# Optimization experiments

Hardware: AMD Instinct MI355X
Metric: run time of the kernel (lower is better)

The kernel has to match this reference:

```python
import jax, jax.numpy as jnp
import numpy as np

B, N, C = 2, 2048, 256
H_DIM, W_DIM = 64, 176


def _lin_init(k, fan_in, shape):
    return jax.random.normal(k, shape, dtype=jnp.float32) * (1.0 / np.sqrt(fan_in))


def setup_inputs() -> dict:
    key = jax.random.key(0)
    ks = jax.random.split(key, 12)
    # gaussian_data: (B, N, 14); positions [:3], sigma_x at 5, sigma_y at 6, weight at 12
    z = jax.random.uniform(ks[0], (B, N), minval=1.0, maxval=40.0)
    x = jax.random.uniform(ks[1], (B, N), minval=-0.6, maxval=0.6) * z
    y = jax.random.uniform(ks[2], (B, N), minval=-0.4, maxval=0.4) * z
    g = jax.random.normal(ks[3], (B, N, 14), dtype=jnp.float32)
    g = g.at[..., 0].set(x).at[..., 1].set(y).at[..., 2].set(z)
    g = g.at[..., 5].set(jax.random.uniform(ks[4], (B, N), minval=5.0, maxval=50.0))
    g = g.at[..., 6].set(jax.random.uniform(ks[5], (B, N), minval=5.0, maxval=50.0))
    g = g.at[..., 12].set(jax.random.uniform(ks[6], (B, N), minval=0.5, maxval=1.5))
    # pinhole intrinsic: fx=fy=1000, cx=880, cy=320
    intrinsic = jnp.array([[1000.0, 0.0, 880.0], [0.0, 1000.0, 320.0], [0.0, 0.0, 1.0]], dtype=jnp.float32)
    pk = jax.random.split(ks[7], 5)
    return {
        "gaussian_data": g,
        "intrinsic": intrinsic,
        "enc_w1": _lin_init(pk[0], 14, (14, 64)), "enc_b1": jnp.zeros((64,), jnp.float32),
        "enc_w2": _lin_init(pk[1], 64, (64, 128)), "enc_b2": jnp.zeros((128,), jnp.float32),
        "enc_w3": _lin_init(pk[2], 128, (128, C)), "enc_b3": jnp.zeros((C,), jnp.float32),
        "ft_w1": _lin_init(pk[3], C, (C, C)), "ft_b1": jnp.zeros((C,), jnp.float32),
        "ft_w2": _lin_init(pk[4], C, (C, C)), "ft_b2": jnp.zeros((C,), jnp.float32),
        "H": H_DIM, "W": W_DIM,
    }


def reference(gaussian_data, intrinsic, enc_w1, enc_b1, enc_w2, enc_b2, enc_w3, enc_b3,
              ft_w1, ft_b1, ft_w2, ft_b2, H, W):
    # Encoder MLP (dropout = identity in eval): (B,N,14) -> (B,N,C)
    h = jax.nn.relu(gaussian_data @ enc_w1 + enc_b1)
    h = jax.nn.relu(h @ enc_w2 + enc_b2)
    feats = h @ enc_w3 + enc_b3
    # feature_transform inside GaussianRadarProjection
    feats_t = jax.nn.relu(feats @ ft_w1 + ft_b1) @ ft_w2 + ft_b2  # (B,N,C)

    pos = gaussian_data[..., :3]                      # (B,N,3)
    valid = pos[..., 2] > 0.1                         # (B,N)
    proj = jnp.einsum('ij,bnj->bni', intrinsic, pos)  # (B,N,3)
    pts2d = proj[..., :2] / (proj[..., 2:3] + 1e-6)   # (B,N,2)
    scale_x = W / intrinsic[0, 2] / 2
    scale_y = H / intrinsic[1, 2] / 2
    px = pts2d[..., 0] * scale_x                      # (B,N)
    py = pts2d[..., 1] * scale_y
    inb = (px >= 0) & (px < W) & (py >= 0) & (py < H)
    mask = valid & inb                                # (B,N)

    sx = jnp.maximum(gaussian_data[..., 5] * scale_x, 1.0)  # (B,N)
    sy = jnp.maximum(gaussian_data[..., 6] * scale_y, 1.0)
    w = gaussian_data[..., 12]                               # (B,N)

    xg = jnp.arange(W, dtype=jnp.float32)
    yg = jnp.arange(H, dtype=jnp.float32)
    dx2 = ((xg[None, None, :] - px[..., None]) / sx[..., None]) ** 2  # (B,N,W)
    dy2 = ((yg[None, None, :] - py[..., None]) / sy[..., None]) ** 2  # (B,N,H)
    dist = dy2[..., :, None] + dx2[..., None, :]                      # (B,N,H,W)
    gw = jnp.exp(-0.5 * dist) * w[..., None, None]
    gw = gw * (dist < 9.0).astype(gw.dtype) * mask[..., None, None].astype(gw.dtype)

    density = jnp.sum(gw, axis=1)[:, None]                             # (B,1,H,W)
    feature_map = jnp.einsum('bnc,bnhw->bchw', feats_t, gw)            # (B,C,H,W)
    avg_sigma = (sx + sy) / 2                                          # (B,N)
    uncertainty = jnp.sum(gw * avg_sigma[..., None, None], axis=1)[:, None]

    density = jnp.clip(density, 1e-6)
    return feature_map / density, uncertainty / density, density
```

## Files before the change

### kernel.cpp

```cpp
#include <hip/hip_runtime.h>
#include <cstdint>
#include <cstddef>

#define B_ 2
#define N_ 2048
#define C_ 256
#define H_ 64
#define W_ 176
#define TW 16
#define NTX 11
#define NYB 32
#define NTILES2 (B_*NYB*NTX)
#define NSUB 8
#define SUBCAP 256
#define SA 260
#define FS 40
#define CSTRIDE 16

typedef unsigned short ushort_t;
typedef short bf16x8 __attribute__((ext_vector_type(8)));
typedef float f32x4  __attribute__((ext_vector_type(4)));

__device__ __forceinline__ short f2bf(float f)
{
    unsigned u = __float_as_uint(f);
    return (short)((u + 0x7FFFu + ((u >> 16) & 1u)) >> 16);
}

__global__ __launch_bounds__(256)
void prep_kernel(const float* __restrict__ w3f, const float* __restrict__ fw1f,
                 const float* __restrict__ fw2f,
                 short* __restrict__ wt3, short* __restrict__ wt4,
                 short* __restrict__ wt5, int* __restrict__ counts)
{
    const int gid = blockIdx.x * 256 + threadIdx.x;
    for (int c = gid; c < NTILES2 * NSUB * CSTRIDE; c += 65536) counts[c] = 0;
    for (int e = gid; e < 163840; e += 65536) {
        if (e < 32768) {
            const int k = e >> 8, n = e & 255;
            wt3[n * 128 + k] = f2bf(w3f[e]);
        } else if (e < 98304) {
            const int e2 = e - 32768;
            const int k = e2 >> 8, n = e2 & 255;
            wt4[n * 256 + k] = f2bf(fw1f[e2]);
        } else {
            const int e2 = e - 98304;
            const int k = e2 >> 8, n = e2 & 255;
            wt5[n * 256 + k] = f2bf(fw2f[e2]);
        }
    }
}

template<int K>
__device__ __forceinline__ void mfma_acc(const short* __restrict__ wt,
                                         const float* actIn, f32x4 (&acc)[2],
                                         int wv_, int quad, int ln15)
{
    bf16x8 wreg[K / 16];
#pragma unroll
    for (int ks = 0; ks < K / 32; ++ks) {
        const int kb = ks * 32 + quad * 8;
#pragma unroll
        for (int tt = 0; tt < 2; ++tt) {
            const int n0 = (wv_ * 2 + tt) * 16;
            wreg[ks * 2 + tt] = *(const bf16x8*)&wt[(size_t)(n0 + ln15) * K + kb];
        }
    }
#pragma unroll
    for (int ks = 0; ks < K / 32; ++ks) {
        const int kb = ks * 32 + quad * 8;
        const float4 a0 = *(const float4*)&actIn[ln15 * SA + kb];
        const float4 a1 = *(const float4*)&actIn[ln15 * SA + kb + 4];
        bf16x8 af = { f2bf(a0.x), f2bf(a0.y), f2bf(a0.z), f2bf(a0.w),
                      f2bf(a1.x), f2bf(a1.y), f2bf(a1.z), f2bf(a1.w) };
#pragma unroll
        for (int tt = 0; tt < 2; ++tt)
            acc[tt] = __builtin_amdgcn_mfma_f32_16x16x32_bf16(af, wreg[ks * 2 + tt],
                                                              acc[tt], 0, 0, 0);
    }
}

__global__ __launch_bounds__(512, 4)
void pb_mlp_kernel(const float* __restrict__ g, const float* __restrict__ intr,
                   const float* __restrict__ w1, const float* __restrict__ b1,
                   const float* __restrict__ w2, const float* __restrict__ b2,
                   const short* __restrict__ wt3, const float* __restrict__ b3,
                   const short* __restrict__ wt4, const float* __restrict__ fb1,
                   const short* __restrict__ wt5, const float* __restrict__ fb2,
                   ushort_t* __restrict__ ftb,
                   float* __restrict__ pp, int* __restrict__ counts,
                   ushort_t* __restrict__ lists)
{
    __shared__ __align__(16) float A_[16 * SA];
    __shared__ __align__(16) float Bb[16 * SA];
    const int tid = threadIdx.x;

    if (blockIdx.x < 256) {
        const int row0 = blockIdx.x * 16;
        const int lane = tid & 63;
        const int wv_  = tid >> 6;
        const int quad = lane >> 4;
        const int ln15 = lane & 15;

        if (tid < 224) {
            const int k = tid / 16, m = tid % 16;
            A_[m * SA + k] = g[(size_t)(row0 + m) * 14 + k];
        }
        __syncthreads();

        {
            const int col = tid & 63;
            const int m0  = (tid >> 6) * 2;
            float acc[2];
            const float bv = b1[col];
            acc[0] = bv; acc[1] = bv;
#pragma unroll
            for (int k = 0; k < 14; ++k) {
                const float wv = w1[k * 64 + col];
                acc[0] = fmaf(A_[(m0 + 0) * SA + k], wv, acc[0]);
                acc[1] = fmaf(A_[(m0 + 1) * SA + k], wv, acc[1]);
            }
            Bb[(m0 + 0) * SA + col] = fmaxf(acc[0], 0.f);
            Bb[(m0 + 1) * SA + col] = fmaxf(acc[1], 0.f);
        }
        __syncthreads();

        {
            const int col = tid & 127;
            const int m0  = (tid >> 7) * 4;
            float acc[4];
            const float bv = b2[col];
#pragma unroll
            for (int r = 0; r < 4; ++r) acc[r] = bv;
#pragma unroll 4
            for (int kq = 0; kq < 16; ++kq) {
                float wv[4];
#pragma unroll
                for (int jj = 0; jj < 4; ++jj) wv[jj] = w2[(4 * kq + jj) * 128 + col];
#pragma unroll
                for (int r = 0; r < 4; ++r) {
                    const float4 a4 = *(const float4*)&Bb[(m0 + r) * SA + 4 * kq];
                    acc[r] = fmaf(a4.x, wv[0], acc[r]);
                    acc[r] = fmaf(a4.y, wv[1], acc[r]);
                    acc[r] = fmaf(a4.z, wv[2], acc[r]);
                    acc[r] = fmaf(a4.w, wv[3], acc[r]);
                }
            }
#pragma unroll
            for (int r = 0; r < 4; ++r)
                A_[(m0 + r) * SA + col] = fmaxf(acc[r], 0.f);
        }
        __syncthreads();

        {
            f32x4 acc[2] = {{0,0,0,0},{0,0,0,0}};
            mfma_acc<128>(wt3, A_, acc, wv_, quad, ln15);
            __syncthreads();
#pragma unroll
            for (int tt = 0; tt < 2; ++tt) {
                const int n = (wv_ * 2 + tt) * 16 + ln15;
                const float bv = b3[n];
#pragma unroll
                for (int r = 0; r < 4; ++r)
                    Bb[(quad * 4 + r) * SA + n] = acc[tt][r] + bv;
            }
        }
        __syncthreads();

        {
            f32x4 acc[2] = {{0,0,0,0},{0,0,0,0}};
            mfma_acc<256>(wt4, Bb, acc, wv_, quad, ln15);
            __syncthreads();
#pragma unroll
            for (int tt = 0; tt < 2; ++tt) {
                const int n = (wv_ * 2 + tt) * 16 + ln15;
                const float bv = fb1[n];
#pragma unroll
                for (int r = 0; r < 4; ++r)
                    A_[(quad * 4 + r) * SA + n] = fmaxf(acc[tt][r] + bv, 0.f);
            }
        }
        __syncthreads();

        {
            f32x4 acc[2] = {{0,0,0,0},{0,0,0,0}};
            mfma_acc<256>(wt5, A_, acc, wv_, quad, ln15);
#pragma unroll
            for (int tt = 0; tt < 2; ++tt) {
                const int n = (wv_ * 2 + tt) * 16 + ln15;
                const float bv = fb2[n];
#pragma unroll
                for (int r = 0; r < 4; ++r)
                    ftb[(size_t)(row0 + quad * 4 + r) * 256 + n] =
                        (ushort_t)f2bf(acc[tt][r] + bv);
            }
        }
        return;
    }

    const int sub = (blockIdx.x - 256) & (NSUB - 1);
    const int i = (blockIdx.x - 256) * 16 + (tid >> 5);
    const int j = tid & 31;
    const float* gi = g + (size_t)i * 14;
    const float x = gi[0], y = gi[1], z = gi[2];
    const float s5 = gi[5], s6 = gi[6], wv = gi[12];
    const float k00 = intr[0], k01 = intr[1], k02 = intr[2];
    const float k10 = intr[3], k11 = intr[4], k12 = intr[5];
    const float k20 = intr[6], k21 = intr[7], k22 = intr[8];
    const float projx = k00 * x + k01 * y + k02 * z;
    const float projy = k10 * x + k11 * y + k12 * z;
    const float projz = k20 * x + k21 * y + k22 * z;
    const float inv = 1.f / (projz + 1e-6f);
    const float scale_x = (float)W_ / k02 * 0.5f;
    const float scale_y = (float)H_ / k12 * 0.5f;
    const float px = projx * inv * scale_x;
    const float py = projy * inv * scale_y;
    const bool valid = z > 0.1f;
    const bool inb = (px >= 0.f) && (px < (float)W_) && (py >= 0.f) && (py < (float)H_);
    const bool mask = valid && inb;
    const float sx = fmaxf(s5 * scale_x, 1.f);
    const float sy = fmaxf(s6 * scale_y, 1.f);
    if (j == 0) {
        float4* o = (float4*)(pp + (size_t)i * 8);
        o[0] = make_float4(px, py, 1.f / sx, 1.f / sy);
        o[1] = make_float4(wv, 0.5f * (sx + sy), 0.f, 0.f);
    }
    if (!mask) return;
    const float rx = 3.f * sx, ry = 3.f * sy;
    const int ymin = max(0, (int)floorf(py - ry));
    const int ymax = min(H_ - 1, (int)ceilf(py + ry));
    const int bmin = ymin >> 1, bmax = ymax >> 1;
    const int band = bmin + j;
    if (band > bmax) return;
    const int tmin = max(0, (int)floorf((px - rx - (float)(TW - 1)) * (1.f / TW)));
    const int tmax = min(NTX - 1, (int)ceilf((px + rx) * (1.f / TW)));
    const int b = i / N_, n = i - b * N_;
    for (int t = tmin; t <= tmax; ++t) {
        const int tile = (b * NYB + band) * NTX + t;
        const int slot = atomicAdd(&counts[(tile * NSUB + sub) * CSTRIDE], 1);
        if (slot < SUBCAP)
            lists[((size_t)tile * NSUB + sub) * SUBCAP + slot] = (ushort_t)n;
    }
}

__global__ __launch_bounds__(256)
void splat_kernel(const float* __restrict__ pp, const ushort_t* __restrict__ lists,
                  const int* __restrict__ counts, const ushort_t* __restrict__ ftb,
                  float* __restrict__ out)
{
    __shared__ __align__(16) ushort_t feats_t[2][256 * FS];
    __shared__ __align__(16) ushort_t gw_t[2][32 * FS];
    __shared__ __align__(16) ushort_t list_s[NSUB * SUBCAP];

    const int tid = threadIdx.x;
    const int qb = blockIdx.x;
    const int b  = qb & 1;
    const int t_ = qb >> 1;
    const int yr = t_ / NTX, xr = t_ % NTX;
    const int yh = (yr + 1) >> 1;
    const int yb = (yr & 1) ? (16 - yh) : (16 + yh);
    const int xh = (xr + 1) >> 1;
    const int txi = (xr & 1) ? (5 - xh) : (5 + xh);
    const int tb  = (b * NYB + yb) * NTX + txi;
    const int y0 = yb * 2, x0 = txi * TW;

    int tot = 0;
#pragma unroll
    for (int s = 0; s < NSUB; ++s) {
        const int cs = min(counts[(tb * NSUB + s) * CSTRIDE], SUBCAP);
        const ushort_t* src = lists + ((size_t)tb * NSUB + s) * SUBCAP;
        for (int k = tid; k < cs; k += 256) list_s[tot + k] = src[k];
        tot += cs;
    }
    __syncthreads();
    const int cnt = tot;

    const ushort_t* mylist = list_s;
    const int gs   = tid >> 5;
    const int px32 = tid & 31;
    const float fy = (float)(y0 + (px32 >> 4));
    const float fx = (float)(x0 + (px32 & 15));
    const int chg = tid >> 4;
    const int qp  = tid & 15;
    const int bN = b * N_;
    const int lane = tid & 63;
    const int wv_  = tid >> 6;
    const int quad = lane >> 4;
    const int ln15 = lane & 15;

    f32x4 acc[2][4];
#pragma unroll
    for (int mt = 0; mt < 2; ++mt)
#pragma unroll
        for (int nt = 0; nt < 4; ++nt) acc[mt][nt] = (f32x4){0.f, 0.f, 0.f, 0.f};
    float densp = 0.f, uncp = 0.f;

    uint4 ra0, ra1, rb0, rb1;
    const int nchunks = (cnt + 31) >> 5;

    if (cnt > 0) {
        const float4* pv = (const float4*)pp;
        {
            const int n0 = mylist[min(2 * qp, cnt - 1)];
            const int n1 = mylist[min(2 * qp + 1, cnt - 1)];
            const uint4* f0 = (const uint4*)(ftb + ((size_t)(bN + n0) << 8) + chg * 16);
            const uint4* f1 = (const uint4*)(ftb + ((size_t)(bN + n1) << 8) + chg * 16);
            ra0 = f0[0]; ra1 = f0[1];
            rb0 = f1[0]; rb1 = f1[1];
        }
        for (int c = 0; c < nchunks; ++c) {
            const int buf = c & 1;
#pragma unroll
            for (int jj = 0; jj < 4; ++jj) {
                const int q = 8 * jj + gs;
                const int qi = c * 32 + q;
                const int n = mylist[min(qi, cnt - 1)];
                const float4 e0 = pv[(size_t)(bN + n) * 2 + 0];
                const float4 e1 = pv[(size_t)(bN + n) * 2 + 1];
                const float dyn = (fy - e0.y) * e0.w;
                const float dxn = (fx - e0.x) * e0.z;
                const float dist = dyn * dyn + dxn * dxn;
                float gv = 0.f;
                if (dist < 9.f) gv = __expf(-0.5f * dist) * e1.x;
                if (qi >= cnt) gv = 0.f;
                gw_t[buf][px32 * FS + q] = (ushort_t)f2bf(gv);
                densp += gv;
                uncp  += gv * e1.y;
            }
            {
                uint* dst = (uint*)&feats_t[buf][0];
#pragma unroll
                for (int jj = 0; jj < 4; ++jj) {
                    const uint u0 = (&ra0.x)[jj], v0 = (&rb0.x)[jj];
                    const int ch = chg * 16 + 2 * jj;
                    dst[ch * (FS / 2) + qp]       = (u0 & 0xffffu) | (v0 << 16);
                    dst[(ch + 1) * (FS / 2) + qp] = (u0 >> 16) | (v0 & 0xffff0000u);
                }
#pragma unroll
                for (int jj = 0; jj < 4; ++jj) {
                    const uint u0 = (&ra1.x)[jj], v0 = (&rb1.x)[jj];
                    const int ch = chg * 16 + 8 + 2 * jj;
                    dst[ch * (FS / 2) + qp]       = (u0 & 0xffffu) | (v0 << 16);
                    dst[(ch + 1) * (FS / 2) + qp] = (u0 >> 16) | (v0 & 0xffff0000u);
                }
            }
            __syncthreads();
            if (c + 1 < nchunks) {
                const int q0 = (c + 1) * 32 + 2 * qp;
                const int n0 = mylist[min(q0, cnt - 1)];
                const int n1 = mylist[min(q0 + 1, cnt - 1)];
                const uint4* f0 = (const uint4*)(ftb + ((size_t)(bN + n0) << 8) + chg * 16);
                const uint4* f1 = (const uint4*)(ftb + ((size_t)(bN + n1) << 8) + chg * 16);
                ra0 = f0[0]; ra1 = f0[1];
                rb0 = f1[0]; rb1 = f1[1];
            }
            bf16x8 af[2];
#pragma unroll
            for (int mt = 0; mt < 2; ++mt)
                af[mt] = *(const bf16x8*)&gw_t[buf][(mt * 16 + ln15) * FS + quad * 8];
#pragma unroll
            for (int nt = 0; nt < 4; ++nt) {
                const int ch0 = wv_ * 64 + nt * 16;
                const bf16x8 bf = *(const bf16x8*)&feats_t[buf][(ch0 + ln15) * FS + quad * 8];
                acc[0][nt] = __builtin_amdgcn_mfma_f32_16x16x32_bf16(af[0], bf, acc[0][nt], 0, 0, 0);
                acc[1][nt] = __builtin_amdgcn_mfma_f32_16x16x32_bf16(af[1], bf, acc[1][nt], 0, 0, 0);
            }
        }
    }

    __syncthreads();
    float* red_d = (float*)&feats_t[0][0];
    float* red_u = red_d + 8 * 36;
    red_d[gs * 36 + px32] = densp;
    red_u[gs * 36 + px32] = uncp;
    __syncthreads();
    for (int s = 4; s > 0; s >>= 1) {
        if (gs < s) {
            red_d[gs * 36 + px32] += red_d[(gs + s) * 36 + px32];
            red_u[gs * 36 + px32] += red_u[(gs + s) * 36 + px32];
        }
        __syncthreads();
    }

    if (tid < 32) {
        const int yy = y0 + (tid >> 4), xx = x0 + (tid & 15);
        const size_t pix = ((size_t)b * H_ + yy) * W_ + xx;
        float* unc_o = out + (size_t)B_ * C_ * H_ * W_;
        float* den_o = unc_o + (size_t)B_ * H_ * W_;
        const float d = fmaxf(red_d[tid], 1e-6f);
        unc_o[pix] = red_u[tid] / d;
        den_o[pix] = d;
    }

#pragma unroll
    for (int mt = 0; mt < 2; ++mt) {
        const int pxb = mt * 16 + quad * 4;
        float rinv[4];
#pragma unroll
        for (int r = 0; r < 4; ++r)
            rinv[r] = 1.f / fmaxf(red_d[pxb + r], 1e-6f);
        const int yy = y0 + mt;
#pragma unroll
        for (int nt = 0; nt < 4; ++nt) {
            const int ch = wv_ * 64 + nt * 16 + ln15;
            float4 v;
            v.x = acc[mt][nt][0] * rinv[0];
            v.y = acc[mt][nt][1] * rinv[1];
            v.z = acc[mt][nt][2] * rinv[2];
            v.w = acc[mt][nt][3] * rinv[3];
            *(float4*)(out + (((size_t)b * C_ + ch) * H_ + yy) * W_
                       + x0 + quad * 4) = v;
        }
    }
}

extern "C" void kernel_launch(void* const* d_in, const int* in_sizes, int n_in,
                              void* d_out, int out_size, void* d_ws, size_t ws_size,
                              hipStream_t stream)
{
    const float* g    = (const float*)d_in[0];
    const float* intr = (const float*)d_in[1];
    const float* w1   = (const float*)d_in[2];
    const float* b1   = (const float*)d_in[3];
    const float* w2   = (const float*)d_in[4];
    const float* b2   = (const float*)d_in[5];
    const float* w3   = (const float*)d_in[6];
    const float* b3   = (const float*)d_in[7];
    const float* fw1  = (const float*)d_in[8];
    const float* fb1  = (const float*)d_in[9];
    const float* fw2  = (const float*)d_in[10];
    const float* fb2  = (const float*)d_in[11];

    char* base = (char*)d_ws;
    const int rows = B_ * N_;
    ushort_t* ftb = (ushort_t*)base;
    float* pp     = (float*)(base + (size_t)rows * C_ * 2);
    int*   counts = (int*)(pp + (size_t)8 * rows);
    ushort_t* lists = (ushort_t*)(counts + NTILES2 * NSUB * CSTRIDE);
    short* wt3    = (short*)(lists + (size_t)NTILES2 * NSUB * SUBCAP);
    short* wt4    = wt3 + 128 * 256;
    short* wt5    = wt4 + 256 * 256;

    prep_kernel<<<dim3(256), dim3(256), 0, stream>>>(w3, fw1, fw2, wt3, wt4, wt5, counts);
    pb_mlp_kernel<<<dim3(512), dim3(512), 0, stream>>>(
        g, intr, w1, b1, w2, b2, wt3, b3, wt4, fb1, wt5, fb2, ftb, pp, counts, lists);
    splat_kernel<<<dim3(NTILES2), dim3(256), 0, stream>>>(pp, lists, counts, ftb, (float*)d_out);
}
```

Before: 133.9 us.

## Double splat block to 512 threads, halving per-thread channel and gaussian work

The splat kernel now launches 512 threads per tile instead of 256. Each wave covers 32 output channels instead of 64, and each thread evaluates 2 gaussians per chunk instead of 4, so per-thread accumulators and feature staging registers are halved. The per-subtile list copy is also unrolled into a single guarded store per thread, which relies on SUBCAP not exceeding the block size. The aim is more resident waves and better latency hiding. The cost is a deeper density reduction tree and more threads contending at each barrier.

```diff
diff --git a/kernel.cpp b/kernel.cpp
--- a/kernel.cpp
+++ b/kernel.cpp
@@ -243,7 +243,7 @@
     }
 }
 
-__global__ __launch_bounds__(256)
+__global__ __launch_bounds__(512)
 void splat_kernel(const float* __restrict__ pp, const ushort_t* __restrict__ lists,
                   const int* __restrict__ counts, const ushort_t* __restrict__ ftb,
                   float* __restrict__ out)
@@ -264,13 +264,18 @@
     const int tb  = (b * NYB + yb) * NTX + txi;
     const int y0 = yb * 2, x0 = txi * TW;
 
+    int cs[NSUB];
+#pragma unroll
+    for (int s = 0; s < NSUB; ++s)
+        cs[s] = min(counts[(tb * NSUB + s) * CSTRIDE], SUBCAP);
+    int off[NSUB];
     int tot = 0;
 #pragma unroll
+    for (int s = 0; s < NSUB; ++s) { off[s] = tot; tot += cs[s]; }
+#pragma unroll
     for (int s = 0; s < NSUB; ++s) {
-        const int cs = min(counts[(tb * NSUB + s) * CSTRIDE], SUBCAP);
         const ushort_t* src = lists + ((size_t)tb * NSUB + s) * SUBCAP;
-        for (int k = tid; k < cs; k += 256) list_s[tot + k] = src[k];
-        tot += cs;
+        if (tid < cs[s]) list_s[off[s] + tid] = src[tid];
     }
     __syncthreads();
     const int cnt = tot;
@@ -288,14 +293,14 @@
     const int quad = lane >> 4;
     const int ln15 = lane & 15;
 
-    f32x4 acc[2][4];
+    f32x4 acc[2][2];
 #pragma unroll
     for (int mt = 0; mt < 2; ++mt)
 #pragma unroll
-        for (int nt = 0; nt < 4; ++nt) acc[mt][nt] = (f32x4){0.f, 0.f, 0.f, 0.f};
+        for (int nt = 0; nt < 2; ++nt) acc[mt][nt] = (f32x4){0.f, 0.f, 0.f, 0.f};
     float densp = 0.f, uncp = 0.f;
 
-    uint4 ra0, ra1, rb0, rb1;
+    uint4 ra0, rb0;
     const int nchunks = (cnt + 31) >> 5;
 
     if (cnt > 0) {
@@ -303,16 +308,14 @@
         {
             const int n0 = mylist[min(2 * qp, cnt - 1)];
             const int n1 = mylist[min(2 * qp + 1, cnt - 1)];
-            const uint4* f0 = (const uint4*)(ftb + ((size_t)(bN + n0) << 8) + chg * 16);
-            const uint4* f1 = (const uint4*)(ftb + ((size_t)(bN + n1) << 8) + chg * 16);
-            ra0 = f0[0]; ra1 = f0[1];
-            rb0 = f1[0]; rb1 = f1[1];
+            ra0 = *(const uint4*)(ftb + ((size_t)(bN + n0) << 8) + chg * 8);
+            rb0 = *(const uint4*)(ftb + ((size_t)(bN + n1) << 8) + chg * 8);
         }
         for (int c = 0; c < nchunks; ++c) {
             const int buf = c & 1;
 #pragma unroll
-            for (int jj = 0; jj < 4; ++jj) {
-                const int q = 8 * jj + gs;
+            for (int jj = 0; jj < 2; ++jj) {
+                const int q = 16 * jj + gs;
                 const int qi = c * 32 + q;
                 const int n = mylist[min(qi, cnt - 1)];
                 const float4 e0 = pv[(size_t)(bN + n) * 2 + 0];
@@ -332,14 +335,7 @@
 #pragma unroll
                 for (int jj = 0; jj < 4; ++jj) {
                     const uint u0 = (&ra0.x)[jj], v0 = (&rb0.x)[jj];
-                    const int ch = chg * 16 + 2 * jj;
-                    dst[ch * (FS / 2) + qp]       = (u0 & 0xffffu) | (v0 << 16);
-                    dst[(ch + 1) * (FS / 2) + qp] = (u0 >> 16) | (v0 & 0xffff0000u);
-                }
-#pragma unroll
-                for (int jj = 0; jj < 4; ++jj) {
-                    const uint u0 = (&ra1.x)[jj], v0 = (&rb1.x)[jj];
-                    const int ch = chg * 16 + 8 + 2 * jj;
+                    const int ch = chg * 8 + 2 * jj;
                     dst[ch * (FS / 2) + qp]       = (u0 & 0xffffu) | (v0 << 16);
                     dst[(ch + 1) * (FS / 2) + qp] = (u0 >> 16) | (v0 & 0xffff0000u);
                 }
@@ -349,18 +345,16 @@
                 const int q0 = (c + 1) * 32 + 2 * qp;
                 const int n0 = mylist[min(q0, cnt - 1)];
                 const int n1 = mylist[min(q0 + 1, cnt - 1)];
-                const uint4* f0 = (const uint4*)(ftb + ((size_t)(bN + n0) << 8) + chg * 16);
-                const uint4* f1 = (const uint4*)(ftb + ((size_t)(bN + n1) << 8) + chg * 16);
-                ra0 = f0[0]; ra1 = f0[1];
-                rb0 = f1[0]; rb1 = f1[1];
+                ra0 = *(const uint4*)(ftb + ((size_t)(bN + n0) << 8) + chg * 8);
+                rb0 = *(const uint4*)(ftb + ((size_t)(bN + n1) << 8) + chg * 8);
             }
             bf16x8 af[2];
 #pragma unroll
             for (int mt = 0; mt < 2; ++mt)
                 af[mt] = *(const bf16x8*)&gw_t[buf][(mt * 16 + ln15) * FS + quad * 8];
 #pragma unroll
-            for (int nt = 0; nt < 4; ++nt) {
-                const int ch0 = wv_ * 64 + nt * 16;
+            for (int nt = 0; nt < 2; ++nt) {
+                const int ch0 = wv_ * 32 + nt * 16;
                 const bf16x8 bf = *(const bf16x8*)&feats_t[buf][(ch0 + ln15) * FS + quad * 8];
                 acc[0][nt] = __builtin_amdgcn_mfma_f32_16x16x32_bf16(af[0], bf, acc[0][nt], 0, 0, 0);
                 acc[1][nt] = __builtin_amdgcn_mfma_f32_16x16x32_bf16(af[1], bf, acc[1][nt], 0, 0, 0);
@@ -370,11 +364,11 @@
 
     __syncthreads();
     float* red_d = (float*)&feats_t[0][0];
-    float* red_u = red_d + 8 * 36;
+    float* red_u = red_d + 16 * 36;
     red_d[gs * 36 + px32] = densp;
     red_u[gs * 36 + px32] = uncp;
     __syncthreads();
-    for (int s = 4; s > 0; s >>= 1) {
+    for (int s = 8; s > 0; s >>= 1) {
         if (gs < s) {
             red_d[gs * 36 + px32] += red_d[(gs + s) * 36 + px32];
             red_u[gs * 36 + px32] += red_u[(gs + s) * 36 + px32];
@@ -401,8 +395,8 @@
             rinv[r] = 1.f / fmaxf(red_d[pxb + r], 1e-6f);
         const int yy = y0 + mt;
 #pragma unroll
-        for (int nt = 0; nt < 4; ++nt) {
-            const int ch = wv_ * 64 + nt * 16 + ln15;
+        for (int nt = 0; nt < 2; ++nt) {
+            const int ch = wv_ * 32 + nt * 16 + ln15;
             float4 v;
             v.x = acc[mt][nt][0] * rinv[0];
             v.y = acc[mt][nt][1] * rinv[1];
@@ -444,5 +438,5 @@
     prep_kernel<<<dim3(256), dim3(256), 0, stream>>>(w3, fw1, fw2, wt3, wt4, wt5, counts);
     pb_mlp_kernel<<<dim3(512), dim3(512), 0, stream>>>(
         g, intr, w1, b1, w2, b2, wt3, b3, wt4, fb1, wt5, fb2, ftb, pp, counts, lists);
-    splat_kernel<<<dim3(NTILES2), dim3(256), 0, stream>>>(pp, lists, counts, ftb, (float*)d_out);
-}
+    splat_kernel<<<dim3(NTILES2), dim3(512), 0, stream>>>(pp, lists, counts, ftb, (float*)d_out);
+}
```

After: 128.8 us. -3.8%, faster.
